# Kernel tuning notes

Hardware: AMD Instinct MI355X
Metric: run time of the kernel (lower is better)

The kernel has to match this reference:

```python
import jax, jax.numpy as jnp
import numpy as np

B, SEQ, EMBED, HEADS = 1, 4096, 4096, 16
HEAD_DIM = EMBED // HEADS  # 256
ROT = 64
MASKED_BIAS = -1e9


def setup_inputs() -> dict:
    key = jax.random.key(0)
    ks = jax.random.split(key, 5)
    s = 0.02
    return {
        "hidden_states": jax.random.normal(ks[0], (B, SEQ, EMBED), jnp.float32),
        "w_q": jax.random.normal(ks[1], (EMBED, EMBED), jnp.float32) * s,
        "w_k": jax.random.normal(ks[2], (EMBED, EMBED), jnp.float32) * s,
        "w_v": jax.random.normal(ks[3], (EMBED, EMBED), jnp.float32) * s,
        "w_out": jax.random.normal(ks[4], (EMBED, EMBED), jnp.float32) * s,
    }


def _rotate_every_two(x):
    # x: [..., rot]; interleave (-x2, x1)
    x1 = x[..., ::2]
    x2 = x[..., 1::2]
    return jnp.stack((-x2, x1), axis=-1).reshape(x.shape)


def _apply_rope(x, sin, cos):
    # x: [B, S, H, ROT]; sin/cos: [S, ROT/2] -> duplicate-interleave to [S, ROT]
    sin = jnp.repeat(sin, 2, axis=-1)[None, :, None, :]
    cos = jnp.repeat(cos, 2, axis=-1)[None, :, None, :]
    return x * cos + _rotate_every_two(x) * sin


def reference(hidden_states, w_q, w_k, w_v, w_out):
    Bt, S, E = hidden_states.shape
    # projections (nn.Linear: x @ W.T)
    q = (hidden_states @ w_q.T).reshape(Bt, S, HEADS, HEAD_DIM)
    k = (hidden_states @ w_k.T).reshape(Bt, S, HEADS, HEAD_DIM)
    v = (hidden_states @ w_v.T).reshape(Bt, S, HEADS, HEAD_DIM)

    # partial rotary embedding on first ROT dims
    inv_freq = 1.0 / (10000.0 ** (jnp.arange(0, ROT, 2, dtype=jnp.float32) / ROT))
    sinusoid = jnp.arange(S, dtype=jnp.float32)[:, None] * inv_freq[None, :]
    sin, cos = jnp.sin(sinusoid), jnp.cos(sinusoid)

    q = jnp.concatenate([_apply_rope(q[..., :ROT], sin, cos), q[..., ROT:]], axis=-1)
    k = jnp.concatenate([_apply_rope(k[..., :ROT], sin, cos), k[..., ROT:]], axis=-1)

    # [B, H, S, D]
    q = q.transpose(0, 2, 1, 3).astype(jnp.float32)
    k = k.transpose(0, 2, 1, 3).astype(jnp.float32)
    v = v.transpose(0, 2, 1, 3)

    # naive fp32 causal attention (mask applied BEFORE scaling, as in source)
    scores = jnp.einsum("bhqd,bhkd->bhqk", q, k)  # [B,H,S,S]
    causal = jnp.tril(jnp.ones((S, S), dtype=bool))[None, None]
    scores = jnp.where(causal, scores, MASKED_BIAS)
    scores = scores / jnp.sqrt(jnp.float32(HEAD_DIM))
    attn = jax.nn.softmax(scores, axis=-1).astype(v.dtype)

    out = jnp.einsum("bhqk,bhkd->bhqd", attn, v)  # [B,H,S,D]
    out = out.transpose(0, 2, 1, 3).reshape(Bt, S, E)
    return out @ w_out.T
```

## Files before the change

kernel.cpp:

```cpp
#include <hip/hip_runtime.h>
#include <cstdint>

#define E 4096
#define SEQL 4096
#define NH 16
#define HD 256

typedef unsigned short u16;
typedef unsigned int u32;
typedef __attribute__((ext_vector_type(8))) short bf16x8;
typedef __attribute__((ext_vector_type(4))) float f32x4;

__device__ __forceinline__ u16 f2bf(float f) {
  union { float f; u32 u; } x; x.f = f;
  u32 r = x.u + 0x7FFFu + ((x.u >> 16) & 1u);
  return (u16)(r >> 16);
}
__device__ __forceinline__ float bf2f(u16 b) {
  union { u32 u; float f; } x; x.u = ((u32)b) << 16; return x.f;
}

__device__ __forceinline__ void gload_lds16(const void* g, void* l) {
  __builtin_amdgcn_global_load_lds((const __attribute__((address_space(1))) void*)g,
                                   (__attribute__((address_space(3))) void*)l, 16, 0, 0);
}

__global__ __launch_bounds__(256) void cast_kernel(const float4* __restrict__ in,
                                                   ushort4* __restrict__ out, int n4) {
  int i = blockIdx.x * 256 + threadIdx.x;
  if (i < n4) {
    float4 v = in[i];
    ushort4 o;
    o.x = f2bf(v.x); o.y = f2bf(v.y); o.z = f2bf(v.z); o.w = f2bf(v.w);
    out[i] = o;
  }
}

__global__ __launch_bounds__(256) void sincos_kernel(float2* __restrict__ sc) {
  int i = blockIdx.x * 256 + threadIdx.x;
  if (i < SEQL * 32) {
    int s = i >> 5, p = i & 31;
    float inv = powf(10000.0f, -(float)p * (1.0f / 32.0f));
    float a = (float)s * inv;
    sc[i] = make_float2(sinf(a), cosf(a));
  }
}

__global__ __launch_bounds__(256) void rope_kernel(u16* __restrict__ q, u16* __restrict__ k,
                                                   const float2* __restrict__ sc) {
  int i = blockIdx.x * 256 + threadIdx.x;
  if (i >= SEQL * NH * 32) return;
  int p = i & 31, h = (i >> 5) & 15, s = i >> 9;
  float2 cs = sc[(s << 5) | p];
  size_t off = ((size_t)s << 12) + ((size_t)h << 8) + ((size_t)p << 1);
  {
    u32* qp = (u32*)(q + off);
    u32 raw = *qp;
    float x0 = bf2f((u16)(raw & 0xFFFFu));
    float x1 = bf2f((u16)(raw >> 16));
    float o0 = x0 * cs.y - x1 * cs.x;
    float o1 = x1 * cs.y + x0 * cs.x;
    *qp = (u32)f2bf(o0) | ((u32)f2bf(o1) << 16);
  }
  {
    u32* kp = (u32*)(k + off);
    u32 raw = *kp;
    float x0 = bf2f((u16)(raw & 0xFFFFu));
    float x1 = bf2f((u16)(raw >> 16));
    float o0 = x0 * cs.y - x1 * cs.x;
    float o1 = x1 * cs.y + x0 * cs.x;
    *kp = (u32)f2bf(o0) | ((u32)f2bf(o1) << 16);
  }
}

template <bool BF16OUT>
__global__ __launch_bounds__(256) void gemm_bt(const u16* __restrict__ A, const u16* __restrict__ B,
                                               void* __restrict__ Cp, int M, int N, int K) {
  __shared__ u16 As[2][128 * 32];
  __shared__ u16 Bs[2][128 * 32];
  const int tid = threadIdx.x, w = tid >> 6, lane = tid & 63;
  const int c15 = lane & 15, q4 = lane >> 4;

  int bid = blockIdx.x;
  int cpx = gridDim.x >> 3;
  int sw = (bid & 7) * cpx + (bid >> 3);
  const int mt = M >> 7;
  const int bm = sw & (mt - 1), bn = sw / mt;
  const int row0 = bm << 7, col0 = bn << 7;
  const int wr = w >> 1, wc = w & 1;

  f32x4 acc[4][4] = {};

  auto stage = [&](int buf, int k0) {
#pragma unroll
    for (int i = 0; i < 2; ++i) {
      int p = w * 128 + i * 64 + lane;
      int r = p >> 2, cph = p & 3;
      int gl = cph ^ ((r >> 1) & 3);
      gload_lds16(A + (size_t)(row0 + r) * K + k0 + gl * 8, &As[buf][(w * 128 + i * 64) * 8]);
      gload_lds16(B + (size_t)(col0 + r) * K + k0 + gl * 8, &Bs[buf][(w * 128 + i * 64) * 8]);
    }
  };

  stage(0, 0);
  const int nt = K >> 5;
  for (int t = 0; t < nt; ++t) {
    const int cur = t & 1;
    __syncthreads();
    if (t + 1 < nt) stage(cur ^ 1, (t + 1) << 5);
    bf16x8 af[4], bfr[4];
#pragma unroll
    for (int m = 0; m < 4; ++m) {
      int ra = wr * 64 + m * 16 + c15;
      int pga = q4 ^ ((ra >> 1) & 3);
      af[m] = *(const bf16x8*)&As[cur][ra * 32 + pga * 8];
      int rb = wc * 64 + m * 16 + c15;
      int pgb = q4 ^ ((rb >> 1) & 3);
      bfr[m] = *(const bf16x8*)&Bs[cur][rb * 32 + pgb * 8];
    }
#pragma unroll
    for (int m = 0; m < 4; ++m)
#pragma unroll
      for (int n = 0; n < 4; ++n)
        acc[m][n] = __builtin_amdgcn_mfma_f32_16x16x32_bf16(af[m], bfr[n], acc[m][n], 0, 0, 0);
  }

#pragma unroll
  for (int m = 0; m < 4; ++m) {
#pragma unroll
    for (int n = 0; n < 4; ++n) {
#pragma unroll
      for (int j = 0; j < 4; ++j) {
        int r = row0 + wr * 64 + m * 16 + q4 * 4 + j;
        int c = col0 + wc * 64 + n * 16 + c15;
        if constexpr (BF16OUT)
          ((u16*)Cp)[(size_t)r * N + c] = f2bf(acc[m][n][j]);
        else
          ((float*)Cp)[(size_t)r * N + c] = acc[m][n][j];
      }
    }
  }
}

__global__ __launch_bounds__(256, 2) void attn_kernel(const u16* __restrict__ Q, const u16* __restrict__ Kt,
                                                      const u16* __restrict__ V, u16* __restrict__ O) {
  __shared__ u16 Ks[64 * 256];
  __shared__ u16 Vt[256 * 64];
  __shared__ u16 Ps[4][16 * 72];

  const int tid = threadIdx.x, w = tid >> 6, lane = tid & 63;
  const int c15 = lane & 15, q4 = lane >> 4;
  const int h = blockIdx.y;
  const int qt = (gridDim.x - 1) - blockIdx.x;
  const int qbase = qt * 64;

  bf16x8 qf[8];
  {
    const u16* qp = Q + (size_t)(qbase + w * 16 + c15) * E + h * HD + q4 * 8;
#pragma unroll
    for (int kc = 0; kc < 8; ++kc) qf[kc] = *(const bf16x8*)(qp + kc * 32);
  }

  f32x4 oacc[16];
#pragma unroll
  for (int i = 0; i < 16; ++i) oacc[i] = f32x4{0.f, 0.f, 0.f, 0.f};
  float mrow[4] = {-3e38f, -3e38f, -3e38f, -3e38f};
  float lrow[4] = {0.f, 0.f, 0.f, 0.f};

  for (int t = 0; t <= qt; ++t) {
    const int kvbase = t * 64;
    __syncthreads();

#pragma unroll
    for (int i = 0; i < 8; ++i) {
      int p = (i * 4 + w) * 64 + lane;
      int r = p >> 5, pg = p & 31;
      int gl = pg ^ ((r & 7) << 2);
      gload_lds16(Kt + (size_t)(kvbase + r) * E + h * HD + gl * 8, &Ks[((i * 4 + w) * 64) * 8]);
    }
#pragma unroll
    for (int i = 0; i < 8; ++i) {
      int d0 = w * 64 + i * 8;
      bf16x8 vv = *(const bf16x8*)(V + (size_t)(kvbase + lane) * E + h * HD + d0);
#pragma unroll
      for (int j = 0; j < 8; ++j) {
        int d = d0 + j;
        int pg = (lane >> 3) ^ ((d >> 1) & 7);
        Vt[d * 64 + pg * 8 + (lane & 7)] = (u16)vv[j];
      }
    }
    __syncthreads();

    f32x4 sacc[4];
#pragma unroll
    for (int n = 0; n < 4; ++n) sacc[n] = f32x4{0.f, 0.f, 0.f, 0.f};
#pragma unroll
    for (int kk = 0; kk < 8; ++kk) {
#pragma unroll
      for (int n = 0; n < 4; ++n) {
        int key = n * 16 + c15;
        int pg5 = (kk * 4 + q4) ^ ((key & 7) << 2);
        bf16x8 kf = *(const bf16x8*)&Ks[key * 256 + pg5 * 8];
        sacc[n] = __builtin_amdgcn_mfma_f32_16x16x32_bf16(qf[kk], kf, sacc[n], 0, 0, 0);
      }
    }

    const bool diag = (t == qt);
#pragma unroll
    for (int n = 0; n < 4; ++n) {
#pragma unroll
      for (int j = 0; j < 4; ++j) {
        float s = sacc[n][j] * 0.0625f;
        if (diag) {
          int key = kvbase + n * 16 + c15;
          int qr = qbase + w * 16 + q4 * 4 + j;
          if (key > qr) s = -3e38f;
        }
        sacc[n][j] = s;
      }
    }

    float rmax[4];
#pragma unroll
    for (int j = 0; j < 4; ++j)
      rmax[j] = fmaxf(fmaxf(sacc[0][j], sacc[1][j]), fmaxf(sacc[2][j], sacc[3][j]));
#pragma unroll
    for (int off = 1; off < 16; off <<= 1)
#pragma unroll
      for (int j = 0; j < 4; ++j) rmax[j] = fmaxf(rmax[j], __shfl_xor(rmax[j], off, 64));

    float mnew[4], scl[4], psum[4];
#pragma unroll
    for (int j = 0; j < 4; ++j) {
      mnew[j] = fmaxf(mrow[j], rmax[j]);
      scl[j] = __expf(mrow[j] - mnew[j]);
      mrow[j] = mnew[j];
      psum[j] = 0.f;
    }

    u16* Pw = &Ps[w][0];
#pragma unroll
    for (int n = 0; n < 4; ++n) {
#pragma unroll
      for (int j = 0; j < 4; ++j) {
        float p = __expf(sacc[n][j] - mnew[j]);
        psum[j] += p;
        Pw[(q4 * 4 + j) * 72 + n * 16 + c15] = f2bf(p);
      }
    }
#pragma unroll
    for (int off = 1; off < 16; off <<= 1)
#pragma unroll
      for (int j = 0; j < 4; ++j) psum[j] += __shfl_xor(psum[j], off, 64);
#pragma unroll
    for (int j = 0; j < 4; ++j) lrow[j] = lrow[j] * scl[j] + psum[j];
#pragma unroll
    for (int i = 0; i < 16; ++i)
#pragma unroll
      for (int j = 0; j < 4; ++j) oacc[i][j] *= scl[j];

    asm volatile("s_waitcnt lgkmcnt(0)" ::: "memory");
    __builtin_amdgcn_sched_barrier(0);

    bf16x8 pf[2];
#pragma unroll
    for (int kkp = 0; kkp < 2; ++kkp)
      pf[kkp] = *(const bf16x8*)(Pw + c15 * 72 + kkp * 32 + q4 * 8);
#pragma unroll
    for (int kkp = 0; kkp < 2; ++kkp) {
#pragma unroll
      for (int n = 0; n < 16; ++n) {
        int d = n * 16 + c15;
        int pg = (kkp * 4 + q4) ^ ((d >> 1) & 7);
        bf16x8 vf = *(const bf16x8*)&Vt[d * 64 + pg * 8];
        oacc[n] = __builtin_amdgcn_mfma_f32_16x16x32_bf16(pf[kkp], vf, oacc[n], 0, 0, 0);
      }
    }
  }

#pragma unroll
  for (int n = 0; n < 16; ++n) {
#pragma unroll
    for (int j = 0; j < 4; ++j) {
      int r = qbase + w * 16 + q4 * 4 + j;
      int c = h * HD + n * 16 + c15;
      O[(size_t)r * E + c] = f2bf(oacc[n][j] / lrow[j]);
    }
  }
}

extern "C" void kernel_launch(void* const* d_in, const int* in_sizes, int n_in,
                              void* d_out, int out_size, void* d_ws, size_t ws_size,
                              hipStream_t stream) {
  const float* hs = (const float*)d_in[0];
  const float* wq = (const float*)d_in[1];
  const float* wk = (const float*)d_in[2];
  const float* wv = (const float*)d_in[3];
  const float* wo = (const float*)d_in[4];
  float* out = (float*)d_out;

  const size_t SZ = (size_t)SEQL * E;
  const size_t SZb = SZ * 2;
  char* ws = (char*)d_ws;
  u16* hs_bf = (u16*)(ws);
  u16* wbuf  = (u16*)(ws + SZb);
  u16* q_bf  = (u16*)(ws + 2 * SZb);
  u16* k_bf  = (u16*)(ws + 3 * SZb);
  u16* v_bf  = (u16*)(ws + 4 * SZb);
  u16* ao_bf = (u16*)(ws + 5 * SZb);
  float2* sc = (float2*)(ws + 6 * SZb);

  const int n4 = (int)(SZ / 4);
  const int cblocks = (n4 + 255) / 256;

  cast_kernel<<<cblocks, 256, 0, stream>>>((const float4*)hs, (ushort4*)hs_bf, n4);
  sincos_kernel<<<(SEQL * 32 + 255) / 256, 256, 0, stream>>>(sc);

  cast_kernel<<<cblocks, 256, 0, stream>>>((const float4*)wq, (ushort4*)wbuf, n4);
  gemm_bt<true><<<1024, 256, 0, stream>>>(hs_bf, wbuf, q_bf, 4096, 4096, 4096);
  cast_kernel<<<cblocks, 256, 0, stream>>>((const float4*)wk, (ushort4*)wbuf, n4);
  gemm_bt<true><<<1024, 256, 0, stream>>>(hs_bf, wbuf, k_bf, 4096, 4096, 4096);
  cast_kernel<<<cblocks, 256, 0, stream>>>((const float4*)wv, (ushort4*)wbuf, n4);
  gemm_bt<true><<<1024, 256, 0, stream>>>(hs_bf, wbuf, v_bf, 4096, 4096, 4096);

  rope_kernel<<<(SEQL * NH * 32 + 255) / 256, 256, 0, stream>>>(q_bf, k_bf, sc);

  attn_kernel<<<dim3(64, 16), 256, 0, stream>>>(q_bf, k_bf, v_bf, ao_bf);

  cast_kernel<<<cblocks, 256, 0, stream>>>((const float4*)wo, (ushort4*)wbuf, n4);
  gemm_bt<false><<<1024, 256, 0, stream>>>(ao_bf, wbuf, out, 4096, 4096, 4096);
}
```

Before: 1.636 ms.

## Write V transposed from GEMM, register-prefetch K/V, and pair causal tiles per block

The V projection GEMM now writes its output transposed to [E, SEQ], so the attention kernel can fill its V^T shared tile with plain vectorized stores instead of a per-element scatter transpose. The attention kernel replaces the async global-to-LDS K load with register double-buffering, loading the next K/V tile into registers while computing on the current one. Each block now handles two query tiles, a long one (63-x) and a short one (x), so the grid is halved and the causal work per block is balanced. The costs are higher register pressure from the 16 int4 prefetch registers plus large accumulators, and uncoalesced transposed 8-byte stores in the V GEMM epilogue.

```diff
diff --git a/kernel.cpp b/kernel.cpp
--- a/kernel.cpp
+++ b/kernel.cpp
@@ -73,7 +73,7 @@
   }
 }
 
-template <bool BF16OUT>
+template <bool BF16OUT, bool TRANSOUT>
 __global__ __launch_bounds__(256) void gemm_bt(const u16* __restrict__ A, const u16* __restrict__ B,
                                                void* __restrict__ Cp, int M, int N, int K) {
   __shared__ u16 As[2][128 * 32];
@@ -129,21 +129,30 @@
   for (int m = 0; m < 4; ++m) {
 #pragma unroll
     for (int n = 0; n < 4; ++n) {
-#pragma unroll
-      for (int j = 0; j < 4; ++j) {
-        int r = row0 + wr * 64 + m * 16 + q4 * 4 + j;
+      if constexpr (TRANSOUT) {
+        int r0 = row0 + wr * 64 + m * 16 + q4 * 4;
         int c = col0 + wc * 64 + n * 16 + c15;
-        if constexpr (BF16OUT)
-          ((u16*)Cp)[(size_t)r * N + c] = f2bf(acc[m][n][j]);
-        else
-          ((float*)Cp)[(size_t)r * N + c] = acc[m][n][j];
-      }
-    }
-  }
-}
-
-__global__ __launch_bounds__(256, 2) void attn_kernel(const u16* __restrict__ Q, const u16* __restrict__ Kt,
-                                                      const u16* __restrict__ V, u16* __restrict__ O) {
+        u32 lo = (u32)f2bf(acc[m][n][0]) | ((u32)f2bf(acc[m][n][1]) << 16);
+        u32 hi = (u32)f2bf(acc[m][n][2]) | ((u32)f2bf(acc[m][n][3]) << 16);
+        uint2 pk; pk.x = lo; pk.y = hi;
+        *(uint2*)((u16*)Cp + (size_t)c * M + r0) = pk;
+      } else {
+#pragma unroll
+        for (int j = 0; j < 4; ++j) {
+          int r = row0 + wr * 64 + m * 16 + q4 * 4 + j;
+          int c = col0 + wc * 64 + n * 16 + c15;
+          if constexpr (BF16OUT)
+            ((u16*)Cp)[(size_t)r * N + c] = f2bf(acc[m][n][j]);
+          else
+            ((float*)Cp)[(size_t)r * N + c] = acc[m][n][j];
+        }
+      }
+    }
+  }
+}
+
+__global__ __launch_bounds__(256, 2) void attn_kernel(const u16* __restrict__ Q, const u16* __restrict__ K,
+                                                      const u16* __restrict__ Vg, u16* __restrict__ O) {
   __shared__ u16 Ks[64 * 256];
   __shared__ u16 Vt[256 * 64];
   __shared__ u16 Ps[4][16 * 72];
@@ -151,140 +160,163 @@
   const int tid = threadIdx.x, w = tid >> 6, lane = tid & 63;
   const int c15 = lane & 15, q4 = lane >> 4;
   const int h = blockIdx.y;
-  const int qt = (gridDim.x - 1) - blockIdx.x;
-  const int qbase = qt * 64;
-
-  bf16x8 qf[8];
-  {
-    const u16* qp = Q + (size_t)(qbase + w * 16 + c15) * E + h * HD + q4 * 8;
-#pragma unroll
-    for (int kc = 0; kc < 8; ++kc) qf[kc] = *(const bf16x8*)(qp + kc * 32);
-  }
-
-  f32x4 oacc[16];
-#pragma unroll
-  for (int i = 0; i < 16; ++i) oacc[i] = f32x4{0.f, 0.f, 0.f, 0.f};
-  float mrow[4] = {-3e38f, -3e38f, -3e38f, -3e38f};
-  float lrow[4] = {0.f, 0.f, 0.f, 0.f};
-
-  for (int t = 0; t <= qt; ++t) {
-    const int kvbase = t * 64;
-    __syncthreads();
+
+  const u16* kb = K + h * HD;
+  const u16* vb = Vg + (size_t)(h * HD) * SEQL;
+
+  int4 kreg[8], vreg[8];
+
+  for (int pass = 0; pass < 2; ++pass) {
+    const int qt = (pass == 0) ? (63 - (int)blockIdx.x) : (int)blockIdx.x;
+    const int qbase = qt * 64;
+
+    bf16x8 qf[8];
+    {
+      const u16* qp = Q + (size_t)(qbase + w * 16 + c15) * E + h * HD + q4 * 8;
+#pragma unroll
+      for (int kc = 0; kc < 8; ++kc) qf[kc] = *(const bf16x8*)(qp + kc * 32);
+    }
+
+    f32x4 oacc[16];
+#pragma unroll
+    for (int i = 0; i < 16; ++i) oacc[i] = f32x4{0.f, 0.f, 0.f, 0.f};
+    float mrow[4] = {-3e38f, -3e38f, -3e38f, -3e38f};
+    float lrow[4] = {0.f, 0.f, 0.f, 0.f};
 
 #pragma unroll
     for (int i = 0; i < 8; ++i) {
-      int p = (i * 4 + w) * 64 + lane;
-      int r = p >> 5, pg = p & 31;
-      int gl = pg ^ ((r & 7) << 2);
-      gload_lds16(Kt + (size_t)(kvbase + r) * E + h * HD + gl * 8, &Ks[((i * 4 + w) * 64) * 8]);
+      int f = i * 256 + tid; int key = f >> 5, c = f & 31;
+      kreg[i] = *(const int4*)(kb + (size_t)key * E + c * 8);
     }
 #pragma unroll
     for (int i = 0; i < 8; ++i) {
-      int d0 = w * 64 + i * 8;
-      bf16x8 vv = *(const bf16x8*)(V + (size_t)(kvbase + lane) * E + h * HD + d0);
-#pragma unroll
-      for (int j = 0; j < 8; ++j) {
-        int d = d0 + j;
-        int pg = (lane >> 3) ^ ((d >> 1) & 7);
-        Vt[d * 64 + pg * 8 + (lane & 7)] = (u16)vv[j];
-      }
-    }
-    __syncthreads();
-
-    f32x4 sacc[4];
-#pragma unroll
-    for (int n = 0; n < 4; ++n) sacc[n] = f32x4{0.f, 0.f, 0.f, 0.f};
-#pragma unroll
-    for (int kk = 0; kk < 8; ++kk) {
+      int f = i * 256 + tid; int d = f >> 3, c = f & 7;
+      vreg[i] = *(const int4*)(vb + (size_t)d * SEQL + c * 8);
+    }
+
+    for (int t = 0; t <= qt; ++t) {
+      const int kvbase = t * 64;
+      __syncthreads();
+#pragma unroll
+      for (int i = 0; i < 8; ++i) {
+        int f = i * 256 + tid; int key = f >> 5, c = f & 31;
+        *(int4*)&Ks[key * 256 + ((c ^ (key & 7)) << 3)] = kreg[i];
+      }
+#pragma unroll
+      for (int i = 0; i < 8; ++i) {
+        int f = i * 256 + tid; int d = f >> 3, c = f & 7;
+        *(int4*)&Vt[(d << 6) + ((c ^ (d & 7)) << 3)] = vreg[i];
+      }
+      __syncthreads();
+      if (t < qt) {
+        const int nb = kvbase + 64;
+#pragma unroll
+        for (int i = 0; i < 8; ++i) {
+          int f = i * 256 + tid; int key = f >> 5, c = f & 31;
+          kreg[i] = *(const int4*)(kb + (size_t)(nb + key) * E + c * 8);
+        }
+#pragma unroll
+        for (int i = 0; i < 8; ++i) {
+          int f = i * 256 + tid; int d = f >> 3, c = f & 7;
+          vreg[i] = *(const int4*)(vb + (size_t)d * SEQL + nb + c * 8);
+        }
+      }
+
+      f32x4 sacc[4];
+#pragma unroll
+      for (int n = 0; n < 4; ++n) sacc[n] = f32x4{0.f, 0.f, 0.f, 0.f};
+#pragma unroll
+      for (int kk = 0; kk < 8; ++kk) {
+#pragma unroll
+        for (int n = 0; n < 4; ++n) {
+          int key = n * 16 + c15;
+          int pg = (kk * 4 + q4) ^ (key & 7);
+          bf16x8 kf = *(const bf16x8*)&Ks[key * 256 + pg * 8];
+          sacc[n] = __builtin_amdgcn_mfma_f32_16x16x32_bf16(qf[kk], kf, sacc[n], 0, 0, 0);
+        }
+      }
+
+      const bool diag = (t == qt);
 #pragma unroll
       for (int n = 0; n < 4; ++n) {
-        int key = n * 16 + c15;
-        int pg5 = (kk * 4 + q4) ^ ((key & 7) << 2);
-        bf16x8 kf = *(const bf16x8*)&Ks[key * 256 + pg5 * 8];
-        sacc[n] = __builtin_amdgcn_mfma_f32_16x16x32_bf16(qf[kk], kf, sacc[n], 0, 0, 0);
-      }
-    }
-
-    const bool diag = (t == qt);
-#pragma unroll
-    for (int n = 0; n < 4; ++n) {
+#pragma unroll
+        for (int j = 0; j < 4; ++j) {
+          float s = sacc[n][j] * 0.0625f;
+          if (diag) {
+            int key = kvbase + n * 16 + c15;
+            int qr = qbase + w * 16 + q4 * 4 + j;
+            if (key > qr) s = -3e38f;
+          }
+          sacc[n][j] = s;
+        }
+      }
+
+      float rmax[4];
+#pragma unroll
+      for (int j = 0; j < 4; ++j)
+        rmax[j] = fmaxf(fmaxf(sacc[0][j], sacc[1][j]), fmaxf(sacc[2][j], sacc[3][j]));
+#pragma unroll
+      for (int off = 1; off < 16; off <<= 1)
+#pragma unroll
+        for (int j = 0; j < 4; ++j) rmax[j] = fmaxf(rmax[j], __shfl_xor(rmax[j], off, 64));
+
+      float mnew[4], scl[4], psum[4];
 #pragma unroll
       for (int j = 0; j < 4; ++j) {
-        float s = sacc[n][j] * 0.0625f;
-        if (diag) {
-          int key = kvbase + n * 16 + c15;
-          int qr = qbase + w * 16 + q4 * 4 + j;
-          if (key > qr) s = -3e38f;
-        }
-        sacc[n][j] = s;
-      }
-    }
-
-    float rmax[4];
-#pragma unroll
-    for (int j = 0; j < 4; ++j)
-      rmax[j] = fmaxf(fmaxf(sacc[0][j], sacc[1][j]), fmaxf(sacc[2][j], sacc[3][j]));
-#pragma unroll
-    for (int off = 1; off < 16; off <<= 1)
-#pragma unroll
-      for (int j = 0; j < 4; ++j) rmax[j] = fmaxf(rmax[j], __shfl_xor(rmax[j], off, 64));
-
-    float mnew[4], scl[4], psum[4];
-#pragma unroll
-    for (int j = 0; j < 4; ++j) {
-      mnew[j] = fmaxf(mrow[j], rmax[j]);
-      scl[j] = __expf(mrow[j] - mnew[j]);
-      mrow[j] = mnew[j];
-      psum[j] = 0.f;
-    }
-
-    u16* Pw = &Ps[w][0];
-#pragma unroll
-    for (int n = 0; n < 4; ++n) {
+        mnew[j] = fmaxf(mrow[j], rmax[j]);
+        scl[j] = __expf(mrow[j] - mnew[j]);
+        mrow[j] = mnew[j];
+        psum[j] = 0.f;
+      }
+
+      u16* Pw = &Ps[w][0];
+#pragma unroll
+      for (int n = 0; n < 4; ++n) {
+#pragma unroll
+        for (int j = 0; j < 4; ++j) {
+          float p = __expf(sacc[n][j] - mnew[j]);
+          psum[j] += p;
+          Pw[(q4 * 4 + j) * 72 + n * 16 + c15] = f2bf(p);
+        }
+      }
+#pragma unroll
+      for (int off = 1; off < 16; off <<= 1)
+#pragma unroll
+        for (int j = 0; j < 4; ++j) psum[j] += __shfl_xor(psum[j], off, 64);
+#pragma unroll
+      for (int j = 0; j < 4; ++j) lrow[j] = lrow[j] * scl[j] + psum[j];
+#pragma unroll
+      for (int i = 0; i < 16; ++i)
+#pragma unroll
+        for (int j = 0; j < 4; ++j) oacc[i][j] *= scl[j];
+
+      asm volatile("s_waitcnt lgkmcnt(0)" ::: "memory");
+      __builtin_amdgcn_sched_barrier(0);
+
+      bf16x8 pf[2];
+#pragma unroll
+      for (int kkp = 0; kkp < 2; ++kkp)
+        pf[kkp] = *(const bf16x8*)(Pw + c15 * 72 + kkp * 32 + q4 * 8);
+#pragma unroll
+      for (int kkp = 0; kkp < 2; ++kkp) {
+#pragma unroll
+        for (int n = 0; n < 16; ++n) {
+          int d = n * 16 + c15;
+          int pg = (kkp * 4 + q4) ^ (d & 7);
+          bf16x8 vf = *(const bf16x8*)&Vt[(d << 6) + pg * 8];
+          oacc[n] = __builtin_amdgcn_mfma_f32_16x16x32_bf16(pf[kkp], vf, oacc[n], 0, 0, 0);
+        }
+      }
+    }
+
+#pragma unroll
+    for (int n = 0; n < 16; ++n) {
 #pragma unroll
       for (int j = 0; j < 4; ++j) {
-        float p = __expf(sacc[n][j] - mnew[j]);
-        psum[j] += p;
-        Pw[(q4 * 4 + j) * 72 + n * 16 + c15] = f2bf(p);
-      }
-    }
-#pragma unroll
-    for (int off = 1; off < 16; off <<= 1)
-#pragma unroll
-      for (int j = 0; j < 4; ++j) psum[j] += __shfl_xor(psum[j], off, 64);
-#pragma unroll
-    for (int j = 0; j < 4; ++j) lrow[j] = lrow[j] * scl[j] + psum[j];
-#pragma unroll
-    for (int i = 0; i < 16; ++i)
-#pragma unroll
-      for (int j = 0; j < 4; ++j) oacc[i][j] *= scl[j];
-
-    asm volatile("s_waitcnt lgkmcnt(0)" ::: "memory");
-    __builtin_amdgcn_sched_barrier(0);
-
-    bf16x8 pf[2];
-#pragma unroll
-    for (int kkp = 0; kkp < 2; ++kkp)
-      pf[kkp] = *(const bf16x8*)(Pw + c15 * 72 + kkp * 32 + q4 * 8);
-#pragma unroll
-    for (int kkp = 0; kkp < 2; ++kkp) {
-#pragma unroll
-      for (int n = 0; n < 16; ++n) {
-        int d = n * 16 + c15;
-        int pg = (kkp * 4 + q4) ^ ((d >> 1) & 7);
-        bf16x8 vf = *(const bf16x8*)&Vt[d * 64 + pg * 8];
-        oacc[n] = __builtin_amdgcn_mfma_f32_16x16x32_bf16(pf[kkp], vf, oacc[n], 0, 0, 0);
-      }
-    }
-  }
-
-#pragma unroll
-  for (int n = 0; n < 16; ++n) {
-#pragma unroll
-    for (int j = 0; j < 4; ++j) {
-      int r = qbase + w * 16 + q4 * 4 + j;
-      int c = h * HD + n * 16 + c15;
-      O[(size_t)r * E + c] = f2bf(oacc[n][j] / lrow[j]);
+        int r = qbase + w * 16 + q4 * 4 + j;
+        int c = h * HD + n * 16 + c15;
+        O[(size_t)r * E + c] = f2bf(oacc[n][j] / lrow[j]);
+      }
     }
   }
 }
@@ -306,7 +338,7 @@
   u16* wbuf  = (u16*)(ws + SZb);
   u16* q_bf  = (u16*)(ws + 2 * SZb);
   u16* k_bf  = (u16*)(ws + 3 * SZb);
-  u16* v_bf  = (u16*)(ws + 4 * SZb);
+  u16* vt_g  = (u16*)(ws + 4 * SZb);
   u16* ao_bf = (u16*)(ws + 5 * SZb);
   float2* sc = (float2*)(ws + 6 * SZb);
 
@@ -317,16 +349,16 @@
   sincos_kernel<<<(SEQL * 32 + 255) / 256, 256, 0, stream>>>(sc);
 
   cast_kernel<<<cblocks, 256, 0, stream>>>((const float4*)wq, (ushort4*)wbuf, n4);
-  gemm_bt<true><<<1024, 256, 0, stream>>>(hs_bf, wbuf, q_bf, 4096, 4096, 4096);
+  gemm_bt<true, false><<<1024, 256, 0, stream>>>(hs_bf, wbuf, q_bf, 4096, 4096, 4096);
   cast_kernel<<<cblocks, 256, 0, stream>>>((const float4*)wk, (ushort4*)wbuf, n4);
-  gemm_bt<true><<<1024, 256, 0, stream>>>(hs_bf, wbuf, k_bf, 4096, 4096, 4096);
+  gemm_bt<true, false><<<1024, 256, 0, stream>>>(hs_bf, wbuf, k_bf, 4096, 4096, 4096);
   cast_kernel<<<cblocks, 256, 0, stream>>>((const float4*)wv, (ushort4*)wbuf, n4);
-  gemm_bt<true><<<1024, 256, 0, stream>>>(hs_bf, wbuf, v_bf, 4096, 4096, 4096);
+  gemm_bt<true, true><<<1024, 256, 0, stream>>>(hs_bf, wbuf, vt_g, 4096, 4096, 4096);
 
   rope_kernel<<<(SEQL * NH * 32 + 255) / 256, 256, 0, stream>>>(q_bf, k_bf, sc);
 
-  attn_kernel<<<dim3(64, 16), 256, 0, stream>>>(q_bf, k_bf, v_bf, ao_bf);
+  attn_kernel<<<dim3(32, 16), 256, 0, stream>>>(q_bf, k_bf, vt_g, ao_bf);
 
   cast_kernel<<<cblocks, 256, 0, stream>>>((const float4*)wo, (ushort4*)wbuf, n4);
-  gemm_bt<false><<<1024, 256, 0, stream>>>(ao_bf, wbuf, out, 4096, 4096, 4096);
-}
+  gemm_bt<false, false><<<1024, 256, 0, stream>>>(ao_bf, wbuf, out, 4096, 4096, 4096);
+}
```

New measurement: 2.071 ms. 26.6% more time.
